# Optimization experiments

Measured on AMD Instinct MI355X. Metric: run time of the kernel, lower is better.

Reference implementation:

```python
import jax, jax.numpy as jnp
import numpy as np


def setup_inputs() -> dict:
    key = jax.random.key(0)
    k0, k1, k2, k3 = jax.random.split(key, 4)
    B, H, W, C, h = 2, 64, 64, 256, 8
    N = H * W
    # per-pixel, per-head (dy, dx) match offsets; a few pixels of displacement
    max_offset = jax.random.normal(k0, (B, N, h, 2), dtype=jnp.float32) * 4.0
    q = jax.random.normal(k1, (B, N, C), dtype=jnp.float32)
    k = jax.random.normal(k2, (B, N, C), dtype=jnp.float32)
    v = jax.random.normal(k3, (B, N, C), dtype=jnp.float32)
    return {"max_offset": max_offset, "q": q, "k": k, "v": v,
            "H": H, "W": W, "r_h": 3, "r_w": 3}


def reference(max_offset, q, k, v, H, W, r_h, r_w):
    """MatchAttention fused forward (l1_norm, scale=1.0).

    Each query pixel (y,x), head g attends to a (2*r_h+1)x(2*r_w+1) window
    centered at (y,x) + round(max_offset[...,g]), clamped to the image.
    Similarity is the negative L1 distance between q and gathered k.
    Returns (output [B,N,C], attn_out [B,N,h,K]).
    """
    B, N, C = q.shape
    h = max_offset.shape[2]
    Ch = C // h
    scale = 1.0
    attn_type = "l1_norm"  # fixed; 'l2_norm' would use squared distance

    # window deltas, K = (2*r_h+1)*(2*r_w+1)
    dy = jnp.arange(-r_h, r_h + 1)
    dx = jnp.arange(-r_w, r_w + 1)
    gy, gx = jnp.meshgrid(dy, dx, indexing="ij")
    ddy, ddx = gy.reshape(-1), gx.reshape(-1)  # [K]

    ys = (jnp.arange(N) // W)[None, :, None]  # [1,N,1]
    xs = (jnp.arange(N) % W)[None, :, None]

    off = jnp.round(max_offset).astype(jnp.int32)  # [B,N,h,2] (dy,dx)
    cy = ys + off[..., 0]                          # [B,N,h] window center
    cx = xs + off[..., 1]
    py = jnp.clip(cy[..., None] + ddy, 0, H - 1)   # [B,N,h,K]
    px = jnp.clip(cx[..., None] + ddx, 0, W - 1)
    idx = py * W + px                              # flat pixel index, [B,N,h,K]

    # split heads and move head axis forward: [B,h,N,Ch]
    qh = q.reshape(B, N, h, Ch).transpose(0, 2, 1, 3)
    kh = k.reshape(B, N, h, Ch).transpose(0, 2, 1, 3)
    vh = v.reshape(B, N, h, Ch).transpose(0, 2, 1, 3)
    idx_t = idx.transpose(0, 2, 1, 3)              # [B,h,N,K]

    # gather windows: [B,h,N,K,Ch]
    gather = jax.vmap(jax.vmap(lambda tbl, i: tbl[i]))
    kg = gather(kh, idx_t)
    vg = gather(vh, idx_t)

    # negative L1 distance similarity, softmax over window
    sim = -scale * jnp.abs(qh[:, :, :, None, :] - kg).sum(-1)  # [B,h,N,K]
    attn = jax.nn.softmax(sim, axis=-1)

    out = jnp.einsum("bhnk,bhnkc->bhnc", attn, vg)
    output = out.transpose(0, 2, 1, 3).reshape(B, N, C)
    attn_out = attn.transpose(0, 2, 1, 3)          # [B,N,h,K]
    return output, attn_out
```

## Files before the change

### kernel.cpp

```cpp
#include <hip/hip_runtime.h>
#include <math.h>

constexpr int B = 2, H = 64, W = 64, C = 256, NH = 8, CH = 32;
constexpr int R = 3, KW = 7, KK = 49, N = H * W;
constexpr int PIX = 32;

template <int CTRL>
static __device__ __forceinline__ float dpp_mov(float v) {
  union { float f; int i; } u;
  u.f = v;
  u.i = __builtin_amdgcn_update_dpp(u.i, u.i, CTRL, 0xf, 0xf, true);
  return u.f;
}
#define DPP_QUAD_XOR1 0xB1
#define DPP_QUAD_XOR2 0x4E
#define DPP_HALF_MIRROR 0x141

__global__ void __launch_bounds__(256, 2) match_attn_kernel(
    const float* __restrict__ moff, const float* __restrict__ qp,
    const float* __restrict__ kp, const float* __restrict__ vp,
    float* __restrict__ outp, float* __restrict__ attnp) {
  const int t = threadIdx.x;
  const int e8 = t & 7;
  const int p = t >> 3;

  const int xcd = blockIdx.x & 7;
  const int rest = blockIdx.x >> 3;
  const int bg = xcd * 2 + (rest >> 7);
  const int slot = rest & 127;
  const int y = slot >> 1;
  const int x = (slot & 1) * PIX + p;
  const int g = bg & 7;
  const int b = bg >> 3;
  const int n = y * W + x;

  const float2 off = *(const float2*)(moff + ((size_t)(b * N + n) * NH + g) * 2);
  const int cy = y + (int)rintf(off.x);
  const int cx = x + (int)rintf(off.y);

  int pxo[KW], pyo[KW];
#pragma unroll
  for (int i = 0; i < KW; ++i) {
    pxo[i] = min(max(cx + i - R, 0), W - 1) << 10;
    pyo[i] = min(max(cy + i - R, 0), H - 1) * (W << 10);
  }
  const int chn = g * CH + e8 * 4;
  const int cb = chn * 4;
  const char* kimg = (const char*)(kp + (size_t)b * N * C);
  const char* vimg = (const char*)(vp + (size_t)b * N * C);

  const float4 q0 = *(const float4*)(qp + (size_t)(b * N + n) * C + chn);

  float ev7[KW];
#pragma unroll
  for (int i = 0; i < KW; ++i) ev7[i] = 0.f;
  float4 acc = {0.f, 0.f, 0.f, 0.f};
  float d0 = 0.f, d1 = 0.f;

  for (int iy = 0; iy < KW; ++iy) {
    const int rowo = cb + pyo[iy];
    float4 kr[KW], vr[KW];
#pragma unroll
    for (int ix = 0; ix < KW; ++ix)
      kr[ix] = *(const float4*)(kimg + (rowo + pxo[ix]));
#pragma unroll
    for (int ix = 0; ix < KW; ++ix)
      vr[ix] = *(const float4*)(vimg + (rowo + pxo[ix]));

    const bool own = (iy == e8);
#pragma unroll
    for (int ix = 0; ix < KW; ++ix) {
      float s = fabsf(q0.x - kr[ix].x) + fabsf(q0.y - kr[ix].y) +
                fabsf(q0.z - kr[ix].z) + fabsf(q0.w - kr[ix].w);
      s += dpp_mov<DPP_QUAD_XOR1>(s);
      s += dpp_mov<DPP_QUAD_XOR2>(s);
      s += dpp_mov<DPP_HALF_MIRROR>(s);
      const float e = __expf(-s);
      if (ix & 1) d1 += e; else d0 += e;
      if (own) ev7[ix] = e;
      acc.x += e * vr[ix].x; acc.y += e * vr[ix].y;
      acc.z += e * vr[ix].z; acc.w += e * vr[ix].w;
    }
  }
  const float inv = 1.0f / (d0 + d1);

  float4 o;
  o.x = acc.x * inv; o.y = acc.y * inv; o.z = acc.z * inv; o.w = acc.w * inv;
  *(float4*)(outp + (size_t)(b * N + n) * C + chn) = o;

  if (e8 < KW) {
    float* attn_row = attnp + ((size_t)(b * N + n) * NH + g) * KK + e8 * KW;
#pragma unroll
    for (int ix = 0; ix < KW; ++ix) attn_row[ix] = ev7[ix] * inv;
  }
}

extern "C" void kernel_launch(void* const* d_in, const int* in_sizes, int n_in,
                              void* d_out, int out_size, void* d_ws, size_t ws_size,
                              hipStream_t stream) {
  const float* moff = (const float*)d_in[0];
  const float* q    = (const float*)d_in[1];
  const float* k    = (const float*)d_in[2];
  const float* v    = (const float*)d_in[3];
  float* out  = (float*)d_out;
  float* attn = out + (size_t)B * N * C;

  const int grid = B * NH * N / PIX;
  match_attn_kernel<<<grid, 256, 0, stream>>>(moff, q, k, v, out, attn);
}
```

Baseline: 116.9 us.

## Pack K and V into interleaved fp16 buffer before windowed attention

```diff
diff --git a/kernel.cpp b/kernel.cpp
--- a/kernel.cpp
+++ b/kernel.cpp
@@ -1,4 +1,5 @@
 #include <hip/hip_runtime.h>
+#include <hip/hip_fp16.h>
 #include <math.h>
 
 constexpr int B = 2, H = 64, W = 64, C = 256, NH = 8, CH = 32;
@@ -16,10 +17,27 @@
 #define DPP_QUAD_XOR2 0x4E
 #define DPP_HALF_MIRROR 0x141
 
+__global__ void __launch_bounds__(256) pack_kv_kernel(
+    const float* __restrict__ kp, const float* __restrict__ vp,
+    __half* __restrict__ kv) {
+  const int idx = blockIdx.x * 256 + threadIdx.x;
+  const int e8 = idx & 7;
+  const int g = (idx >> 3) & 7;
+  const int bn = idx >> 6;
+  const float4 kf = *(const float4*)(kp + (size_t)bn * C + g * CH + e8 * 4);
+  const float4 vf = *(const float4*)(vp + (size_t)bn * C + g * CH + e8 * 4);
+  __half2 o[4];
+  o[0] = __floats2half2_rn(kf.x, kf.y);
+  o[1] = __floats2half2_rn(kf.z, kf.w);
+  o[2] = __floats2half2_rn(vf.x, vf.y);
+  o[3] = __floats2half2_rn(vf.z, vf.w);
+  *(float4*)(kv + ((size_t)(bn * NH + g) * 64 + e8 * 8)) = *(float4*)o;
+}
+
 __global__ void __launch_bounds__(256, 2) match_attn_kernel(
     const float* __restrict__ moff, const float* __restrict__ qp,
-    const float* __restrict__ kp, const float* __restrict__ vp,
-    float* __restrict__ outp, float* __restrict__ attnp) {
+    const __half* __restrict__ kvp, float* __restrict__ outp,
+    float* __restrict__ attnp) {
   const int t = threadIdx.x;
   const int e8 = t & 7;
   const int p = t >> 3;
@@ -38,18 +56,19 @@
   const int cy = y + (int)rintf(off.x);
   const int cx = x + (int)rintf(off.y);
 
-  int pxo[KW], pyo[KW];
+  int pxo[KW], rowo[KW];
 #pragma unroll
   for (int i = 0; i < KW; ++i) {
     pxo[i] = min(max(cx + i - R, 0), W - 1) << 10;
-    pyo[i] = min(max(cy + i - R, 0), H - 1) * (W << 10);
+    rowo[i] = min(max(cy + i - R, 0), H - 1) << 16;
   }
+  const char* kvimg = (const char*)kvp +
+      (size_t)b * N * NH * 128 + g * 128 + e8 * 16;
+
   const int chn = g * CH + e8 * 4;
-  const int cb = chn * 4;
-  const char* kimg = (const char*)(kp + (size_t)b * N * C);
-  const char* vimg = (const char*)(vp + (size_t)b * N * C);
-
   const float4 q0 = *(const float4*)(qp + (size_t)(b * N + n) * C + chn);
+  const __half2 q01 = __floats2half2_rn(q0.x, q0.y);
+  const __half2 q23 = __floats2half2_rn(q0.z, q0.w);
 
   float ev7[KW];
 #pragma unroll
@@ -57,29 +76,32 @@
   float4 acc = {0.f, 0.f, 0.f, 0.f};
   float d0 = 0.f, d1 = 0.f;
 
+  union KV { float4 f; __half2 h[4]; };
   for (int iy = 0; iy < KW; ++iy) {
-    const int rowo = cb + pyo[iy];
-    float4 kr[KW], vr[KW];
+    const int ro = rowo[iy];
+    KV kv[KW];
 #pragma unroll
     for (int ix = 0; ix < KW; ++ix)
-      kr[ix] = *(const float4*)(kimg + (rowo + pxo[ix]));
-#pragma unroll
-    for (int ix = 0; ix < KW; ++ix)
-      vr[ix] = *(const float4*)(vimg + (rowo + pxo[ix]));
+      kv[ix].f = *(const float4*)(kvimg + (ro + pxo[ix]));
 
     const bool own = (iy == e8);
 #pragma unroll
     for (int ix = 0; ix < KW; ++ix) {
-      float s = fabsf(q0.x - kr[ix].x) + fabsf(q0.y - kr[ix].y) +
-                fabsf(q0.z - kr[ix].z) + fabsf(q0.w - kr[ix].w);
+      const __half2 d01h = __habs2(__hsub2(q01, kv[ix].h[0]));
+      const __half2 d23h = __habs2(__hsub2(q23, kv[ix].h[1]));
+      const float2 f01 = __half22float2(d01h);
+      const float2 f23 = __half22float2(d23h);
+      float s = (f01.x + f01.y) + (f23.x + f23.y);
       s += dpp_mov<DPP_QUAD_XOR1>(s);
       s += dpp_mov<DPP_QUAD_XOR2>(s);
       s += dpp_mov<DPP_HALF_MIRROR>(s);
       const float e = __expf(-s);
       if (ix & 1) d1 += e; else d0 += e;
       if (own) ev7[ix] = e;
-      acc.x += e * vr[ix].x; acc.y += e * vr[ix].y;
-      acc.z += e * vr[ix].z; acc.w += e * vr[ix].w;
+      const float2 v01 = __half22float2(kv[ix].h[2]);
+      const float2 v23 = __half22float2(kv[ix].h[3]);
+      acc.x += e * v01.x; acc.y += e * v01.y;
+      acc.z += e * v23.x; acc.w += e * v23.y;
     }
   }
   const float inv = 1.0f / (d0 + d1);
@@ -104,7 +126,9 @@
   const float* v    = (const float*)d_in[3];
   float* out  = (float*)d_out;
   float* attn = out + (size_t)B * N * C;
+  __half* kv = (__half*)d_ws;
 
+  pack_kv_kernel<<<B * N * NH * 8 / 256, 256, 0, stream>>>(k, v, kv);
   const int grid = B * NH * N / PIX;
-  match_attn_kernel<<<grid, 256, 0, stream>>>(moff, q, k, v, out, attn);
+  match_attn_kernel<<<grid, 256, 0, stream>>>(moff, q, kv, out, attn);
 }
```

Result: no change. 116.2 us (-0.5%).
